# Kernel tuning notes

Hardware: AMD Instinct MI355X
Metric: run time of the kernel (lower is better)

The kernel has to match this reference:

```python
import jax, jax.numpy as jnp
import numpy as np

D = 1024      # model dim
H = 16        # heads
DH = 64       # dim per head (lucidrains default)
DEPTH = 6
MLP = 2048
P = 32
PD = 3 * P * P   # 3072
NC = 1000
B = 4         # packed sequences
N = 640       # tokens per packed sequence (incl. padding)
M = 18        # images per packed sequence
GRID = 8      # image_size // patch_size
SIZES = [(8,8),(8,8),(7,7),(7,7),(6,8),(8,6),(6,6),(5,7),(7,5),(5,5),(4,8),(8,4),(4,6),(6,4),(4,4),(3,5),(5,3),(3,3)]
SCALE = DH ** -0.5


def _pack_meta():
    hs, ws, ids = [], [], []
    for i, (h, w) in enumerate(SIZES):
        hh, ww = np.meshgrid(np.arange(h), np.arange(w), indexing='ij')
        hs.append(hh.ravel()); ws.append(ww.ravel()); ids.append(np.full(h * w, i))
    h = np.concatenate(hs); w = np.concatenate(ws); ii = np.concatenate(ids)
    pad = N - h.shape[0]
    h = np.pad(h, (0, pad)); w = np.pad(w, (0, pad))
    ii = np.pad(ii, (0, pad), constant_values=-1)  # padding tokens form their own block
    return (np.tile(h, (B, 1)).astype(np.int32),
            np.tile(w, (B, 1)).astype(np.int32),
            np.tile(ii, (B, 1)).astype(np.int32))


def _ln(x, g, b, eps=1e-5):
    m = x.mean(-1, keepdims=True)
    v = ((x - m) ** 2).mean(-1, keepdims=True)
    return (x - m) * jax.lax.rsqrt(v + eps) * g + b


def _heads(t):  # [b, n, H*DH] -> [b, H, n, DH]
    return t.reshape(t.shape[0], t.shape[1], H, DH).swapaxes(1, 2)


def _mha(q_in, kv_in, mask, Wq, Wkv, Wo, qn_g, qn_b, kn_g, kn_b):
    # NaViT attention: pre-norm applied by caller to q_in; per-head qk LayerNorm; no biases.
    q = _ln(_heads(q_in @ Wq), qn_g, qn_b)
    k, v = jnp.split(kv_in @ Wkv, 2, axis=-1)
    k = _ln(_heads(k), kn_g, kn_b)
    v = _heads(v)
    dots = jnp.einsum('bhid,bhjd->bhij', q, k) * SCALE
    dots = jnp.where(mask, dots, jnp.finfo(dots.dtype).min)
    o = jnp.einsum('bhij,bhjd->bhid', jax.nn.softmax(dots, axis=-1), v)
    o = o.swapaxes(1, 2).reshape(o.shape[0], -1, H * DH)
    return o @ Wo


def _forward(patches, pe_ln1_g, pe_ln1_b, W_pe, b_pe, pe_ln2_g, pe_ln2_b, pos_h, pos_w,
             ln1_g, ln1_b, qn_g, qn_b, kn_g, kn_b, Wq, Wkv, Wo, ln2_g, ln2_b,
             W1, b1, W2, b2, fin_g, fin_b, pool_q, pl_ln_g, pl_ln_b, pl_qn_g, pl_qn_b,
             pl_kn_g, pl_kn_b, pl_Wq, pl_Wkv, pl_Wo, head_g, head_b, W_head, b_head,
             h_idx, w_idx, image_ids):
    # patch embedding: LN -> Linear -> LN, then factorized 2D pos embed
    x = _ln(patches, pe_ln1_g, pe_ln1_b) @ W_pe + b_pe
    x = _ln(x, pe_ln2_g, pe_ln2_b)
    x = x + pos_h[h_idx] + pos_w[w_idx]
    # block-diagonal attention mask: tokens attend only within their own image
    blk = (image_ids[:, :, None] == image_ids[:, None, :])[:, None]  # [B,1,N,N]
    for l in range(DEPTH):
        xn = _ln(x, ln1_g[l], ln1_b[l])
        x = x + _mha(xn, xn, blk, Wq[l], Wkv[l], Wo[l], qn_g[l], qn_b[l], kn_g[l], kn_b[l])
        xn = _ln(x, ln2_g[l], ln2_b[l])
        x = x + jax.nn.gelu(xn @ W1[l] + b1[l], approximate=False) @ W2[l] + b2[l]
    x = _ln(x, fin_g, fin_b)
    # attention pooling: one learned query per packed image (context NOT re-normed, as in na_vit)
    queries = jnp.broadcast_to(pool_q, (B, M, D))
    qn = _ln(queries, pl_ln_g, pl_ln_b)
    pmask = (jnp.arange(M)[None, :, None] == image_ids[:, None, :])[:, None]  # [B,1,M,N]
    pooled = _mha(qn, x, pmask, pl_Wq, pl_Wkv, pl_Wo, pl_qn_g, pl_qn_b, pl_kn_g, pl_kn_b) + queries
    pooled = pooled.reshape(B * M, D)
    return _ln(pooled, head_g, head_b) @ W_head + b_head  # [B*M, 1000]


def setup_inputs() -> dict:
    key = jax.random.key(0)
    ks = iter(jax.random.split(key, 32))
    h_idx, w_idx, image_ids = _pack_meta()
    f32 = jnp.float32
    d = dict(
        patches=jax.random.normal(next(ks), (B, N, PD), f32),
        pe_ln1_g=jnp.ones((PD,), f32), pe_ln1_b=jnp.zeros((PD,), f32),
        W_pe=0.02 * jax.random.normal(next(ks), (PD, D), f32), b_pe=jnp.zeros((D,), f32),
        pe_ln2_g=jnp.ones((D,), f32), pe_ln2_b=jnp.zeros((D,), f32),
        pos_h=0.02 * jax.random.normal(next(ks), (GRID, D), f32),
        pos_w=0.02 * jax.random.normal(next(ks), (GRID, D), f32),
        ln1_g=jnp.ones((DEPTH, D), f32), ln1_b=jnp.zeros((DEPTH, D), f32),
        qn_g=jnp.ones((DEPTH, DH), f32), qn_b=jnp.zeros((DEPTH, DH), f32),
        kn_g=jnp.ones((DEPTH, DH), f32), kn_b=jnp.zeros((DEPTH, DH), f32),
        Wq=0.02 * jax.random.normal(next(ks), (DEPTH, D, H * DH), f32),
        Wkv=0.02 * jax.random.normal(next(ks), (DEPTH, D, 2 * H * DH), f32),
        Wo=0.02 * jax.random.normal(next(ks), (DEPTH, H * DH, D), f32),
        ln2_g=jnp.ones((DEPTH, D), f32), ln2_b=jnp.zeros((DEPTH, D), f32),
        W1=0.02 * jax.random.normal(next(ks), (DEPTH, D, MLP), f32), b1=jnp.zeros((DEPTH, MLP), f32),
        W2=0.02 * jax.random.normal(next(ks), (DEPTH, MLP, D), f32), b2=jnp.zeros((DEPTH, D), f32),
        fin_g=jnp.ones((D,), f32), fin_b=jnp.zeros((D,), f32),
        pool_q=0.02 * jax.random.normal(next(ks), (D,), f32),
        pl_ln_g=jnp.ones((D,), f32), pl_ln_b=jnp.zeros((D,), f32),
        pl_qn_g=jnp.ones((DH,), f32), pl_qn_b=jnp.zeros((DH,), f32),
        pl_kn_g=jnp.ones((DH,), f32), pl_kn_b=jnp.zeros((DH,), f32),
        pl_Wq=0.02 * jax.random.normal(next(ks), (D, H * DH), f32),
        pl_Wkv=0.02 * jax.random.normal(next(ks), (D, 2 * H * DH), f32),
        pl_Wo=0.02 * jax.random.normal(next(ks), (H * DH, D), f32),
        head_g=jnp.ones((D,), f32), head_b=jnp.zeros((D,), f32),
        W_head=0.02 * jax.random.normal(next(ks), (D, NC), f32), b_head=jnp.zeros((NC,), f32),
        h_idx=jnp.asarray(h_idx), w_idx=jnp.asarray(w_idx), image_ids=jnp.asarray(image_ids),
    )
    return d


def reference(patches, pe_ln1_g, pe_ln1_b, W_pe, b_pe, pe_ln2_g, pe_ln2_b, pos_h, pos_w,
              ln1_g, ln1_b, qn_g, qn_b, kn_g, kn_b, Wq, Wkv, Wo, ln2_g, ln2_b,
              W1, b1, W2, b2, fin_g, fin_b, pool_q, pl_ln_g, pl_ln_b, pl_qn_g, pl_qn_b,
              pl_kn_g, pl_kn_b, pl_Wq, pl_Wkv, pl_Wo, head_g, head_b, W_head, b_head,
              h_idx, w_idx, image_ids):
    return _forward(patches, pe_ln1_g, pe_ln1_b, W_pe, b_pe, pe_ln2_g, pe_ln2_b, pos_h, pos_w,
                    ln1_g, ln1_b, qn_g, qn_b, kn_g, kn_b, Wq, Wkv, Wo, ln2_g, ln2_b,
                    W1, b1, W2, b2, fin_g, fin_b, pool_q, pl_ln_g, pl_ln_b, pl_qn_g, pl_qn_b,
                    pl_kn_g, pl_kn_b, pl_Wq, pl_Wkv, pl_Wo, head_g, head_b, W_head, b_head,
                    h_idx, w_idx, image_ids)
```

## Files before the change

### kernel.cpp

```cpp
#include <hip/hip_runtime.h>
#include <cmath>

constexpr int kB = 4, kN = 640, kD = 1024, kH = 16, kDH = 64;
constexpr int kDepth = 6, kMLP = 2048, kPD = 3072, kNC = 1000, kM = 18;
constexpr float kScale = 0.125f;
constexpr float kNegInf = -3.4028235e38f;

typedef __bf16 bf16;
typedef __attribute__((ext_vector_type(8))) __bf16 bf16x8;
typedef __attribute__((ext_vector_type(4))) __bf16 bf16x4;
typedef __attribute__((ext_vector_type(4))) float f32x4;

#define AS1 __attribute__((address_space(1)))
#define AS3 __attribute__((address_space(3)))

__device__ __forceinline__ void gload16(const void* g, void* l) {
  __builtin_amdgcn_global_load_lds((AS1 void*)g, (AS3 void*)l, 16, 0, 0);
}

constexpr size_t kMEG = 1048576;
constexpr size_t kOffPe = 0;
constexpr size_t kLayer0 = 3 * kMEG;
constexpr size_t kLayerSz = 8 * kMEG;
constexpr size_t kOffPool = kLayer0 + 6 * kLayerSz;
constexpr size_t kOffPlWq = kOffPool;
constexpr size_t kOffPlWkv = kOffPool + 1 * kMEG;
constexpr size_t kOffPlWo = kOffPool + 3 * kMEG;
constexpr size_t kOffHead = kOffPool + 4 * kMEG;

__global__ __launch_bounds__(256) void wt_all_kernel(
    const float* __restrict__ pe, const float* __restrict__ wq,
    const float* __restrict__ wkv, const float* __restrict__ wo,
    const float* __restrict__ w1, const float* __restrict__ w2,
    const float* __restrict__ plq, const float* __restrict__ plkv,
    const float* __restrict__ plo, const float* __restrict__ whead,
    bf16* __restrict__ WTB) {
  const int j = blockIdx.y;
  const float* W;
  size_t doff;
  int K, Nc, Np;
  if (j == 0) {
    W = pe; K = 3072; Nc = 1024; Np = 1024; doff = kOffPe;
  } else if (j < 31) {
    const int l = (j - 1) / 5, w = (j - 1) % 5;
    const size_t lbase = kLayer0 + (size_t)l * kLayerSz;
    switch (w) {
      case 0:  W = wq  + (size_t)l * kMEG;     K = 1024; Nc = 1024; doff = lbase;            break;
      case 1:  W = wkv + (size_t)l * 2 * kMEG; K = 1024; Nc = 2048; doff = lbase + kMEG;     break;
      case 2:  W = wo  + (size_t)l * kMEG;     K = 1024; Nc = 1024; doff = lbase + 3 * kMEG; break;
      case 3:  W = w1  + (size_t)l * 2 * kMEG; K = 1024; Nc = 2048; doff = lbase + 4 * kMEG; break;
      default: W = w2  + (size_t)l * 2 * kMEG; K = 2048; Nc = 1024; doff = lbase + 6 * kMEG; break;
    }
    Np = Nc;
  } else if (j == 31) { W = plq;  K = 1024; Nc = 1024; Np = 1024; doff = kOffPlWq; }
  else if (j == 32)   { W = plkv; K = 1024; Nc = 2048; Np = 2048; doff = kOffPlWkv; }
  else if (j == 33)   { W = plo;  K = 1024; Nc = 1024; Np = 1024; doff = kOffPlWo; }
  else                { W = whead; K = 1024; Nc = 1000; Np = 1024; doff = kOffHead; }
  const int nbx = Np >> 6;
  const int ntiles = nbx * (K >> 6);
  const int tile = blockIdx.x;
  if (tile >= ntiles) return;
  const int n0 = (tile % nbx) * 64, k0 = (tile / nbx) * 64;
  bf16* WT = WTB + doff;
  __shared__ float s[64][65];
  const int tid = threadIdx.x;
  if (n0 + 64 <= Nc) {
#pragma unroll
    for (int i = 0; i < 4; ++i) {
      const int c = i * 256 + tid;
      const int r = c >> 4, cq = c & 15;
      const float4 v = *(const float4*)(W + (size_t)(k0 + r) * Nc + n0 + cq * 4);
      s[r][cq * 4 + 0] = v.x; s[r][cq * 4 + 1] = v.y;
      s[r][cq * 4 + 2] = v.z; s[r][cq * 4 + 3] = v.w;
    }
  } else {
#pragma unroll
    for (int i = 0; i < 4; ++i) {
      const int c = i * 256 + tid;
      const int r = c >> 4, cq = c & 15;
#pragma unroll
      for (int e = 0; e < 4; ++e) {
        const int n = n0 + cq * 4 + e;
        s[r][cq * 4 + e] = (n < Nc) ? W[(size_t)(k0 + r) * Nc + n] : 0.f;
      }
    }
  }
  __syncthreads();
#pragma unroll
  for (int i = 0; i < 2; ++i) {
    const int c = i * 256 + tid;
    const int n = c >> 3, kq = c & 7;
    bf16x8 w;
#pragma unroll
    for (int e = 0; e < 8; ++e) w[e] = (bf16)s[kq * 8 + e][n];
    *(bf16x8*)(WT + (size_t)(n0 + n) * K + k0 + kq * 8) = w;
  }
}

template <typename OT>
__global__ __launch_bounds__(256) void ln_kernel(
    const float* __restrict__ in, OT* __restrict__ out,
    const float* __restrict__ g, const float* __restrict__ b, int K) {
  const int row = blockIdx.x;
  const float* x = in + (size_t)row * K;
  OT* o = out + (size_t)row * K;
  const int K4 = K >> 2;
  float s = 0.f, s2 = 0.f;
  for (int c = threadIdx.x; c < K4; c += 256) {
    const float4 v = ((const float4*)x)[c];
    s += v.x + v.y + v.z + v.w;
    s2 += v.x * v.x + v.y * v.y + v.z * v.z + v.w * v.w;
  }
#pragma unroll
  for (int off = 32; off; off >>= 1) { s += __shfl_down(s, off); s2 += __shfl_down(s2, off); }
  __shared__ float ls[4], ls2[4];
  __shared__ float sm, sr;
  const int wid = threadIdx.x >> 6, lane = threadIdx.x & 63;
  if (lane == 0) { ls[wid] = s; ls2[wid] = s2; }
  __syncthreads();
  if (threadIdx.x == 0) {
    float a = ls[0] + ls[1] + ls[2] + ls[3];
    float a2 = ls2[0] + ls2[1] + ls2[2] + ls2[3];
    float mean = a / K;
    float var = a2 / K - mean * mean;
    sm = mean; sr = rsqrtf(var + 1e-5f);
  }
  __syncthreads();
  const float mean = sm, r = sr;
  for (int c = threadIdx.x; c < K4; c += 256) {
    const float4 v = ((const float4*)x)[c];
    const float4 gv = ((const float4*)g)[c];
    const float4 bv = ((const float4*)b)[c];
    const int d = c * 4;
    o[d + 0] = (OT)((v.x - mean) * r * gv.x + bv.x);
    o[d + 1] = (OT)((v.y - mean) * r * gv.y + bv.y);
    o[d + 2] = (OT)((v.z - mean) * r * gv.z + bv.z);
    o[d + 3] = (OT)((v.w - mean) * r * gv.w + bv.w);
  }
}

__global__ __launch_bounds__(256) void ln_pos_kernel(
    const float* __restrict__ in, float* __restrict__ out,
    const float* __restrict__ g, const float* __restrict__ b,
    const float* __restrict__ ph, const float* __restrict__ pw,
    const int* __restrict__ hi, const int* __restrict__ wi) {
  const int row = blockIdx.x;
  const float* x = in + (size_t)row * kD;
  float* o = out + (size_t)row * kD;
  const int c = threadIdx.x;
  const float4 v = ((const float4*)x)[c];
  float s = v.x + v.y + v.z + v.w;
  float s2 = v.x * v.x + v.y * v.y + v.z * v.z + v.w * v.w;
#pragma unroll
  for (int off = 32; off; off >>= 1) { s += __shfl_down(s, off); s2 += __shfl_down(s2, off); }
  __shared__ float ls[4], ls2[4];
  __shared__ float sm, sr;
  const int wid = threadIdx.x >> 6, lane = threadIdx.x & 63;
  if (lane == 0) { ls[wid] = s; ls2[wid] = s2; }
  __syncthreads();
  if (threadIdx.x == 0) {
    float a = ls[0] + ls[1] + ls[2] + ls[3];
    float a2 = ls2[0] + ls2[1] + ls2[2] + ls2[3];
    float mean = a / kD;
    float var = a2 / kD - mean * mean;
    sm = mean; sr = rsqrtf(var + 1e-5f);
  }
  __syncthreads();
  const float mean = sm, r = sr;
  const float4* phr = (const float4*)(ph + (size_t)hi[row] * kD);
  const float4* pwr = (const float4*)(pw + (size_t)wi[row] * kD);
  const float4 gv = ((const float4*)g)[c];
  const float4 bv = ((const float4*)b)[c];
  const float4 hv = phr[c], wv = pwr[c];
  float4 ov;
  ov.x = (v.x - mean) * r * gv.x + bv.x + hv.x + wv.x;
  ov.y = (v.y - mean) * r * gv.y + bv.y + hv.y + wv.y;
  ov.z = (v.z - mean) * r * gv.z + bv.z + hv.z + wv.z;
  ov.w = (v.w - mean) * r * gv.w + bv.w + hv.w + wv.w;
  ((float4*)o)[c] = ov;
}

__global__ __launch_bounds__(256) void poolq_kernel(
    const float* __restrict__ pq, const float* __restrict__ lg,
    const float* __restrict__ lb, const bf16* __restrict__ WqT,
    const float* __restrict__ qg, const float* __restrict__ qb,
    float* __restrict__ qpool) {
  const int h = blockIdx.x, tid = threadIdx.x;
  __shared__ float qs[1024];
  __shared__ float red[256];
  __shared__ float ls[4], ls2[4];
  __shared__ float sm, sr;
  const float4 v = ((const float4*)pq)[tid];
  float s = v.x + v.y + v.z + v.w;
  float s2 = v.x * v.x + v.y * v.y + v.z * v.z + v.w * v.w;
#pragma unroll
  for (int off = 32; off; off >>= 1) { s += __shfl_down(s, off); s2 += __shfl_down(s2, off); }
  const int wid = tid >> 6, lane = tid & 63;
  if (lane == 0) { ls[wid] = s; ls2[wid] = s2; }
  __syncthreads();
  if (tid == 0) {
    float a = ls[0] + ls[1] + ls[2] + ls[3];
    float a2 = ls2[0] + ls2[1] + ls2[2] + ls2[3];
    float mean = a / kD;
    sm = mean; sr = rsqrtf(a2 / kD - mean * mean + 1e-5f);
  }
  __syncthreads();
  {
    const float mean = sm, r = sr;
    const float4 gv = ((const float4*)lg)[tid];
    const float4 bv = ((const float4*)lb)[tid];
    qs[tid * 4 + 0] = (v.x - mean) * r * gv.x + bv.x;
    qs[tid * 4 + 1] = (v.y - mean) * r * gv.y + bv.y;
    qs[tid * 4 + 2] = (v.z - mean) * r * gv.z + bv.z;
    qs[tid * 4 + 3] = (v.w - mean) * r * gv.w + bv.w;
  }
  __syncthreads();
  const int d = tid & 63, qq = tid >> 6;
  const bf16* wrow = WqT + (size_t)(h * 64 + d) * 1024 + qq * 256;
  const float* qp = qs + qq * 256;
  float part = 0.f;
  for (int k = 0; k < 256; k += 8) {
    const bf16x8 w8 = *(const bf16x8*)(wrow + k);
#pragma unroll
    for (int e = 0; e < 8; ++e) part += qp[k + e] * (float)w8[e];
  }
  red[tid] = part;
  __syncthreads();
  if (tid < 64) {
    const float dot = red[tid] + red[tid + 64] + red[tid + 128] + red[tid + 192];
    float hs = dot, hs2 = dot * dot;
#pragma unroll
    for (int off = 32; off; off >>= 1) { hs += __shfl_xor(hs, off); hs2 += __shfl_xor(hs2, off); }
    const float m = hs * (1.f / kDH);
    const float r = rsqrtf(hs2 * (1.f / kDH) - m * m + 1e-5f);
    qpool[h * 64 + tid] = (dot - m) * r * qg[tid] + qb[tid];
  }
}

template <int NI, bool OUT_BF, bool GELU, bool HLN>
__global__ __launch_bounds__(256) void gemm64_kernel(
    const bf16* __restrict__ A, const bf16* __restrict__ WT,
    float* __restrict__ Cf, bf16* __restrict__ Cb,
    const float* __restrict__ bias, const float* __restrict__ res,
    const float* __restrict__ hg, const float* __restrict__ hb,
    int K, int Ncol, int nbx) {
  constexpr int BN = NI * 32;
  __shared__ __align__(16) bf16 As[2][64 * 64];
  __shared__ __align__(16) bf16 Bs[2][BN * 64];
  const int tid = threadIdx.x, lane = tid & 63, wid = tid >> 6;
  const int wr = wid >> 1, wc = wid & 1;
  const int cpx = gridDim.x >> 3;
  const int swz = (blockIdx.x & 7) * cpx + (blockIdx.x >> 3);
  const int row0 = (swz / nbx) * 64, col0 = (swz % nbx) * BN;
  const int fr = lane & 15, fg = lane >> 4;
  f32x4 acc[2][NI] = {};
  bf16* sA = As[0]; bf16* sB = Bs[0];
  bf16* dA = As[1]; bf16* dB = Bs[1];

  auto stage = [&](bf16* tA, bf16* tB, int kt) {
#pragma unroll
    for (int i = 0; i < 2; ++i) {
      const int c = i * 256 + tid;
      const int r = c >> 3, ci = c & 7;
      gload16(A + (size_t)(row0 + r) * K + kt + ((ci ^ (r & 7)) * 8),
              tA + (i * 256 + wid * 64) * 8);
    }
#pragma unroll
    for (int i = 0; i < NI; ++i) {
      const int c = i * 256 + tid;
      const int r = c >> 3, ci = c & 7;
      gload16(WT + (size_t)(col0 + r) * K + kt + ((ci ^ (r & 7)) * 8),
              tB + (i * 256 + wid * 64) * 8);
    }
  };
  auto compute = [&](const bf16* tA, const bf16* tB) {
#pragma unroll
    for (int kk = 0; kk < 2; ++kk) {
      bf16x8 af[2], bfr[NI];
#pragma unroll
      for (int mi = 0; mi < 2; ++mi) {
        const int r = wr * 32 + mi * 16 + fr;
        af[mi] = *(const bf16x8*)(tA + r * 64 + (((kk * 4 + fg) ^ (r & 7)) * 8));
      }
#pragma unroll
      for (int ni = 0; ni < NI; ++ni) {
        const int r = wc * (NI * 16) + ni * 16 + fr;
        bfr[ni] = *(const bf16x8*)(tB + r * 64 + (((kk * 4 + fg) ^ (r & 7)) * 8));
      }
#pragma unroll
      for (int mi = 0; mi < 2; ++mi)
#pragma unroll
        for (int ni = 0; ni < NI; ++ni)
          acc[mi][ni] = __builtin_amdgcn_mfma_f32_16x16x32_bf16(af[mi], bfr[ni], acc[mi][ni], 0, 0, 0);
    }
  };

  const int NT = K >> 6;
  stage(sA, sB, 0);
  __syncthreads();
  for (int t = 1; t < NT; ++t) {
    stage(dA, dB, t * 64);
    compute(sA, sB);
    __syncthreads();
    bf16* u;
    u = sA; sA = dA; dA = u;
    u = sB; sB = dB; dB = u;
  }
  compute(sA, sB);

  const int rb = row0 + wr * 32 + fg * 4;
  const int cb = col0 + wc * (NI * 16) + fr;
  float hm[2][4], hr[2][4];
  if (HLN) {
#pragma unroll
    for (int mi = 0; mi < 2; ++mi)
#pragma unroll
      for (int r = 0; r < 4; ++r) {
        float s = 0.f, s2 = 0.f;
#pragma unroll
        for (int ni = 0; ni < NI; ++ni) {
          const float v = acc[mi][ni][r];
          s += v; s2 += v * v;
        }
#pragma unroll
        for (int off = 1; off < 16; off <<= 1) {
          s += __shfl_xor(s, off); s2 += __shfl_xor(s2, off);
        }
        const float m = s * (1.f / kDH);
        hm[mi][r] = m;
        hr[mi][r] = rsqrtf(s2 * (1.f / kDH) - m * m + 1e-5f);
      }
  }
  const bool kHalf = HLN && (cb < kD);
#pragma unroll
  for (int mi = 0; mi < 2; ++mi) {
#pragma unroll
    for (int ni = 0; ni < NI; ++ni) {
      const int cc = cb + ni * 16;
      const float bb = bias ? bias[cc] : 0.f;
      const float hgv = HLN ? hg[ni * 16 + fr] : 0.f;
      const float hbv = HLN ? hb[ni * 16 + fr] : 0.f;
#pragma unroll
      for (int r = 0; r < 4; ++r) {
        const int rr = rb + mi * 16 + r;
        float v = acc[mi][ni][r] + bb;
        if (res) v += res[(size_t)rr * Ncol + cc];
        if (GELU) v = 0.5f * v * (1.f + erff(v * 0.70710678118654752f));
        if (HLN && kHalf) v = (v - hm[mi][r]) * hr[mi][r] * hgv + hbv;
        if (OUT_BF) Cb[(size_t)rr * Ncol + cc] = (bf16)v;
        else        Cf[(size_t)rr * Ncol + cc] = v;
      }
    }
  }
}

template <bool OUT_BF>
__global__ __launch_bounds__(256) void gemm_tail_kernel(
    const bf16* __restrict__ A, const bf16* __restrict__ WT,
    float* __restrict__ Cf, bf16* __restrict__ Cb,
    const float* __restrict__ bias, const float* __restrict__ resv,
    int Mr, int K, int Nc, int ldc, int resmode) {
  __shared__ __align__(16) bf16 As[64][40];
  __shared__ __align__(16) bf16 Bs[128][40];
  const int tid = threadIdx.x;
  const int lane = tid & 63, wid = tid >> 6;
  const int row0 = blockIdx.y * 64, col0 = blockIdx.x * 128;
  f32x4 acc[4][2] = {};
  const int am = tid >> 2, ako = (tid & 3) * 8;
  const int fr = lane & 15, fg = (lane >> 4) * 8;
  for (int k0 = 0; k0 < K; k0 += 32) {
    if (row0 + am < Mr)
      *(bf16x8*)&As[am][ako] = *(const bf16x8*)(A + (size_t)(row0 + am) * K + k0 + ako);
    else {
      bf16x8 z = {};
      *(bf16x8*)&As[am][ako] = z;
    }
#pragma unroll
    for (int it = 0; it < 2; ++it) {
      const int c = it * 256 + tid;
      const int n = c >> 2, ko = (c & 3) * 8;
      *(bf16x8*)&Bs[n][ko] = *(const bf16x8*)(WT + (size_t)(col0 + n) * K + k0 + ko);
    }
    __syncthreads();
    bf16x8 af[4], bfr[2];
#pragma unroll
    for (int mi = 0; mi < 4; ++mi) af[mi] = *(const bf16x8*)&As[mi * 16 + fr][fg];
#pragma unroll
    for (int ni = 0; ni < 2; ++ni) bfr[ni] = *(const bf16x8*)&Bs[wid * 32 + ni * 16 + fr][fg];
#pragma unroll
    for (int mi = 0; mi < 4; ++mi)
#pragma unroll
      for (int ni = 0; ni < 2; ++ni)
        acc[mi][ni] = __builtin_amdgcn_mfma_f32_16x16x32_bf16(af[mi], bfr[ni], acc[mi][ni], 0, 0, 0);
    __syncthreads();
  }
  const int r4 = (lane >> 4) * 4;
  const int cc0 = col0 + wid * 32 + (lane & 15);
#pragma unroll
  for (int mi = 0; mi < 4; ++mi) {
#pragma unroll
    for (int ni = 0; ni < 2; ++ni) {
      const int cc = cc0 + ni * 16;
      if (cc >= Nc) continue;
#pragma unroll
      for (int r = 0; r < 4; ++r) {
        const int rr = row0 + mi * 16 + r4 + r;
        if (rr >= Mr) continue;
        float v = acc[mi][ni][r];
        if (bias) v += bias[cc];
        if (resmode == 1) v += resv[(size_t)rr * ldc + cc];
        else if (resmode == 2) v += resv[cc];
        if (OUT_BF) Cb[(size_t)rr * ldc + cc] = (bf16)v;
        else        Cf[(size_t)rr * ldc + cc] = v;
      }
    }
  }
}

__global__ __launch_bounds__(256) void attn_kernel(
    const bf16* __restrict__ qkv, const int* __restrict__ ids,
    const float* __restrict__ qg, const float* __restrict__ qb,
    const float* __restrict__ kg, const float* __restrict__ kb,
    bf16* __restrict__ o) {
  const int h = blockIdx.x, img = blockIdx.y, b = blockIdx.z;
  const int tid = threadIdx.x, lane = tid & 63, wid = tid >> 6;
  __shared__ __align__(16) bf16 Qs[64][72];
  __shared__ __align__(16) bf16 Ks[64][72];
  __shared__ __align__(16) bf16 Vt[64][72];
  __shared__ __align__(16) bf16 Ps[64][72];
  __shared__ int wlo[4], whi[4];
  __shared__ int sLo, sHi;
  {
    const int want = (img < kM) ? img : -1;
    int lo = kN, hi = -1;
    for (int j = tid; j < kN; j += 256) {
      if (ids[b * kN + j] == want) { lo = min(lo, j); hi = max(hi, j); }
    }
#pragma unroll
    for (int off = 32; off; off >>= 1) {
      lo = min(lo, __shfl_xor(lo, off));
      hi = max(hi, __shfl_xor(hi, off));
    }
    if (lane == 0) { wlo[wid] = lo; whi[wid] = hi; }
    __syncthreads();
    if (tid == 0) {
      sLo = min(min(wlo[0], wlo[1]), min(wlo[2], wlo[3]));
      sHi = max(max(whi[0], whi[1]), max(whi[2], whi[3]));
    }
    __syncthreads();
  }
  if (sHi < 0) return;
  const int start = sLo, T = sHi - sLo + 1;
  if (img == kM) {
    for (int j = start + wid; j <= sHi; j += 4)
      o[((size_t)(b * kN + j)) * kD + h * kDH + lane] = (bf16)0.f;
    return;
  }
#pragma unroll
  for (int it = 0; it < 2; ++it) {
    const int ch = it * 256 + tid;
    const int r = ch >> 3, d0 = (ch & 7) * 8;
    if (r < T) {
      const bf16* base = qkv + ((size_t)(b * kN + start + r)) * 3072 + h * kDH + d0;
      const bf16x8 qv = *(const bf16x8*)(base);
      const bf16x8 kv = *(const bf16x8*)(base + 1024);
      const bf16x8 vv = *(const bf16x8*)(base + 2048);
      float qf[8], kf[8];
      float sq = 0.f, sq2 = 0.f, sk = 0.f, sk2 = 0.f;
#pragma unroll
      for (int e = 0; e < 8; ++e) {
        qf[e] = (float)qv[e]; kf[e] = (float)kv[e];
        sq += qf[e]; sq2 += qf[e] * qf[e];
        sk += kf[e]; sk2 += kf[e] * kf[e];
      }
#pragma unroll
      for (int off = 1; off < 8; off <<= 1) {
        sq += __shfl_xor(sq, off); sq2 += __shfl_xor(sq2, off);
        sk += __shfl_xor(sk, off); sk2 += __shfl_xor(sk2, off);
      }
      const float qm = sq * (1.f / 64);
      const float qr = rsqrtf(sq2 * (1.f / 64) - qm * qm + 1e-5f);
      const float km = sk * (1.f / 64);
      const float kr = rsqrtf(sk2 * (1.f / 64) - km * km + 1e-5f);
      bf16x8 qw, kw;
#pragma unroll
      for (int e = 0; e < 8; ++e) {
        qw[e] = (bf16)((qf[e] - qm) * qr * qg[d0 + e] + qb[d0 + e]);
        kw[e] = (bf16)((kf[e] - km) * kr * kg[d0 + e] + kb[d0 + e]);
      }
      *(bf16x8*)&Qs[r][d0] = qw;
      *(bf16x8*)&Ks[r][d0] = kw;
#pragma unroll
      for (int e = 0; e < 8; ++e) Vt[d0 + e][r] = vv[e];
    } else {
      const bf16x8 z = {};
      *(bf16x8*)&Qs[r][d0] = z;
      *(bf16x8*)&Ks[r][d0] = z;
#pragma unroll
      for (int e = 0; e < 8; ++e) Vt[d0 + e][r] = (bf16)0.f;
    }
  }
  __syncthreads();
  const int fr = lane & 15, fg = lane >> 4;
  const int r0 = wid * 16;
  f32x4 sacc[4] = {};
#pragma unroll
  for (int k0 = 0; k0 < 64; k0 += 32) {
    const bf16x8 aq = *(const bf16x8*)&Qs[r0 + fr][k0 + fg * 8];
#pragma unroll
    for (int ni = 0; ni < 4; ++ni) {
      const bf16x8 bk = *(const bf16x8*)&Ks[ni * 16 + fr][k0 + fg * 8];
      sacc[ni] = __builtin_amdgcn_mfma_f32_16x16x32_bf16(aq, bk, sacc[ni], 0, 0, 0);
    }
  }
  float inv[4];
#pragma unroll
  for (int r = 0; r < 4; ++r) {
    float mx = kNegInf;
#pragma unroll
    for (int ni = 0; ni < 4; ++ni) {
      const float s = (ni * 16 + fr < T) ? sacc[ni][r] * kScale : kNegInf;
      sacc[ni][r] = s;
      mx = fmaxf(mx, s);
    }
#pragma unroll
    for (int off = 1; off < 16; off <<= 1) mx = fmaxf(mx, __shfl_xor(mx, off));
    float sum = 0.f;
#pragma unroll
    for (int ni = 0; ni < 4; ++ni) {
      const float p = __expf(sacc[ni][r] - mx);
      sacc[ni][r] = p;
      sum += p;
    }
#pragma unroll
    for (int off = 1; off < 16; off <<= 1) sum += __shfl_xor(sum, off);
    inv[r] = 1.f / sum;
  }
#pragma unroll
  for (int ni = 0; ni < 4; ++ni)
#pragma unroll
    for (int r = 0; r < 4; ++r)
      Ps[r0 + fg * 4 + r][ni * 16 + fr] = (bf16)sacc[ni][r];
  f32x4 oacc[4] = {};
#pragma unroll
  for (int k0 = 0; k0 < 64; k0 += 32) {
    const bf16x8 ap = *(const bf16x8*)&Ps[r0 + fr][k0 + fg * 8];
#pragma unroll
    for (int ni = 0; ni < 4; ++ni) {
      const bf16x8 bv = *(const bf16x8*)&Vt[ni * 16 + fr][k0 + fg * 8];
      oacc[ni] = __builtin_amdgcn_mfma_f32_16x16x32_bf16(ap, bv, oacc[ni], 0, 0, 0);
    }
  }
#pragma unroll
  for (int r = 0; r < 4; ++r) {
    const int i = r0 + fg * 4 + r;
    if (i < T) {
      const size_t orow = ((size_t)(b * kN + start + i)) * kD + h * kDH;
      const float iv = inv[r];
#pragma unroll
      for (int ni = 0; ni < 4; ++ni)
        o[orow + ni * 16 + fr] = (bf16)(oacc[ni][r] * iv);
    }
  }
}

__global__ __launch_bounds__(64) void poolattn_kernel(
    const float* __restrict__ qp, const bf16* __restrict__ kv,
    const int* __restrict__ ids, bf16* __restrict__ o) {
  const int blk = blockIdx.x;
  const int h = blk % kH;
  const int bm = blk / kH;
  const int m = bm % kM, b = bm / kM;
  const int lane = threadIdx.x;
  __shared__ float sc[kN];
  __shared__ float qs[kDH];
  qs[lane] = qp[h * kDH + lane];
  __syncthreads();
  float mymax = kNegInf;
  int jmn = kN, jmx = -1;
  for (int j = lane; j < kN; j += 64) {
    const int idj = ids[b * kN + j];
    float s;
    if (idj == m) {
      const bf16* krow = kv + ((size_t)(b * kN + j)) * (2 * kD) + h * kDH;
      float dot = 0.f;
#pragma unroll
      for (int d = 0; d < kDH; ++d) dot += qs[d] * (float)krow[d];
      s = dot * kScale;
      jmn = min(jmn, j); jmx = max(jmx, j);
    } else {
      s = kNegInf;
    }
    sc[j] = s;
    mymax = fmaxf(mymax, s);
  }
#pragma unroll
  for (int off = 32; off; off >>= 1) {
    mymax = fmaxf(mymax, __shfl_xor(mymax, off));
    jmn = min(jmn, __shfl_xor(jmn, off));
    jmx = max(jmx, __shfl_xor(jmx, off));
  }
  const int jlo = jmn, jhi = jmx + 1;
  float mysum = 0.f;
  for (int j = jlo + lane; j < jhi; j += 64) {
    const float p = __expf(sc[j] - mymax);
    sc[j] = p;
    mysum += p;
  }
#pragma unroll
  for (int off = 32; off; off >>= 1) mysum += __shfl_xor(mysum, off);
  const float inv = 1.f / mysum;
  __syncthreads();
  float acc = 0.f;
  const bf16* vptr = kv + ((size_t)(b * kN + jlo)) * (2 * kD) + kD + h * kDH + lane;
  for (int j = jlo; j < jhi; ++j, vptr += 2 * kD) acc += sc[j] * (float)vptr[0];
  o[((size_t)(b * kM + m)) * kD + h * kDH + lane] = (bf16)(acc * inv);
}

extern "C" void kernel_launch(void* const* d_in, const int* in_sizes, int n_in,
                              void* d_out, int out_size, void* d_ws, size_t ws_size,
                              hipStream_t stream) {
  const float* patches  = (const float*)d_in[0];
  const float* pe_ln1_g = (const float*)d_in[1];
  const float* pe_ln1_b = (const float*)d_in[2];
  const float* W_pe     = (const float*)d_in[3];
  const float* b_pe     = (const float*)d_in[4];
  const float* pe_ln2_g = (const float*)d_in[5];
  const float* pe_ln2_b = (const float*)d_in[6];
  const float* pos_h    = (const float*)d_in[7];
  const float* pos_w    = (const float*)d_in[8];
  const float* ln1_g    = (const float*)d_in[9];
  const float* ln1_b    = (const float*)d_in[10];
  const float* qn_g     = (const float*)d_in[11];
  const float* qn_b     = (const float*)d_in[12];
  const float* kn_g     = (const float*)d_in[13];
  const float* kn_b     = (const float*)d_in[14];
  const float* Wq       = (const float*)d_in[15];
  const float* Wkv      = (const float*)d_in[16];
  const float* Wo       = (const float*)d_in[17];
  const float* ln2_g    = (const float*)d_in[18];
  const float* ln2_b    = (const float*)d_in[19];
  const float* W1       = (const float*)d_in[20];
  const float* b1       = (const float*)d_in[21];
  const float* W2       = (const float*)d_in[22];
  const float* b2       = (const float*)d_in[23];
  const float* fin_g    = (const float*)d_in[24];
  const float* fin_b    = (const float*)d_in[25];
  const float* pool_q   = (const float*)d_in[26];
  const float* pl_ln_g  = (const float*)d_in[27];
  const float* pl_ln_b  = (const float*)d_in[28];
  const float* pl_qn_g  = (const float*)d_in[29];
  const float* pl_qn_b  = (const float*)d_in[30];
  const float* pl_kn_g  = (const float*)d_in[31];
  const float* pl_kn_b  = (const float*)d_in[32];
  const float* pl_Wq    = (const float*)d_in[33];
  const float* pl_Wkv   = (const float*)d_in[34];
  const float* pl_Wo    = (const float*)d_in[35];
  const float* head_g   = (const float*)d_in[36];
  const float* head_b   = (const float*)d_in[37];
  const float* W_head   = (const float*)d_in[38];
  const float* b_head   = (const float*)d_in[39];
  const int* h_idx      = (const int*)d_in[40];
  const int* w_idx      = (const int*)d_in[41];
  const int* image_ids  = (const int*)d_in[42];
  float* out = (float*)d_out;

  const size_t SZ = (size_t)kB * kN * kD;
  char* p = (char*)d_ws;
  float* x    = (float*)p;           p += SZ * 4;
  bf16*  xnb  = (bf16*)p;            p += SZ * 2;
  char*  scratch = p;                p += 32u * 1024 * 1024;
  char*  smalls = p;                 p += 1u * 1024 * 1024;
  bf16*  wtbuf = (bf16*)p;
  bf16*  qkvbb = (bf16*)scratch;
  bf16*  attno = (bf16*)(scratch + 16u * 1024 * 1024);
  bf16*  plnb  = (bf16*)scratch;
  float* emb   = (float*)(scratch + 16u * 1024 * 1024);
  bf16*  h1b   = (bf16*)scratch;
  bf16*  kvpoolb = (bf16*)scratch;
  float* qpool   = (float*)smalls;
  bf16*  opoolb  = (bf16*)(smalls + 8192);
  float* pooled  = (float*)(smalls + 8192 + 163840);
  bf16*  pooledn = (bf16*)(smalls + 8192 + 163840 + 327680);

  const int BN = kB * kN;
  const int nbyM = BN / 64;

  wt_all_kernel<<<dim3(768, 35), 256, 0, stream>>>(
      W_pe, Wq, Wkv, Wo, W1, W2, pl_Wq, pl_Wkv, pl_Wo, W_head, wtbuf);

  ln_kernel<bf16><<<BN, 256, 0, stream>>>(patches, plnb, pe_ln1_g, pe_ln1_b, kPD);
  gemm64_kernel<2, false, false, false><<<(kD / 64) * nbyM, 256, 0, stream>>>(
      plnb, wtbuf + kOffPe, emb, nullptr, b_pe, nullptr, nullptr, nullptr, kPD, kD, kD / 64);
  ln_pos_kernel<<<BN, 256, 0, stream>>>(emb, x, pe_ln2_g, pe_ln2_b, pos_h, pos_w, h_idx, w_idx);

  for (int l = 0; l < kDepth; ++l) {
    const bf16* lw = wtbuf + kLayer0 + (size_t)l * kLayerSz;
    ln_kernel<bf16><<<BN, 256, 0, stream>>>(x, xnb, ln1_g + (size_t)l * kD, ln1_b + (size_t)l * kD, kD);
    gemm64_kernel<2, true, false, false><<<(3 * kD / 64) * nbyM, 256, 0, stream>>>(
        xnb, lw, nullptr, qkvbb, nullptr, nullptr, nullptr, nullptr, kD, 3 * kD, 3 * kD / 64);
    attn_kernel<<<dim3(kH, kM + 1, kB), 256, 0, stream>>>(
        qkvbb, image_ids,
        qn_g + (size_t)l * kDH, qn_b + (size_t)l * kDH,
        kn_g + (size_t)l * kDH, kn_b + (size_t)l * kDH, attno);
    gemm64_kernel<2, false, false, false><<<(kD / 64) * nbyM, 256, 0, stream>>>(
        attno, lw + 3 * kMEG, x, nullptr, nullptr, x, nullptr, nullptr, kD, kD, kD / 64);
    ln_kernel<bf16><<<BN, 256, 0, stream>>>(x, xnb, ln2_g + (size_t)l * kD, ln2_b + (size_t)l * kD, kD);
    gemm64_kernel<2, true, true, false><<<(kMLP / 64) * nbyM, 256, 0, stream>>>(
        xnb, lw + 4 * kMEG, nullptr, h1b, b1 + (size_t)l * kMLP, nullptr, nullptr, nullptr, kD, kMLP, kMLP / 64);
    gemm64_kernel<2, false, false, false><<<(kD / 64) * nbyM, 256, 0, stream>>>(
        h1b, lw + 6 * kMEG, x, nullptr, b2 + (size_t)l * kD, x, nullptr, nullptr, kMLP, kD, kD / 64);
  }

  ln_kernel<bf16><<<BN, 256, 0, stream>>>(x, xnb, fin_g, fin_b, kD);

  poolq_kernel<<<kH, 256, 0, stream>>>(
      pool_q, pl_ln_g, pl_ln_b, wtbuf + kOffPlWq, pl_qn_g, pl_qn_b, qpool);
  gemm64_kernel<4, true, false, true><<<(2 * kD / 128) * nbyM, 256, 0, stream>>>(
      xnb, wtbuf + kOffPlWkv, nullptr, kvpoolb, nullptr, nullptr, pl_kn_g, pl_kn_b, kD, 2 * kD, 2 * kD / 128);
  poolattn_kernel<<<kB * kM * kH, 64, 0, stream>>>(qpool, kvpoolb, image_ids, opoolb);
  gemm_tail_kernel<false><<<dim3(8, 2), 256, 0, stream>>>(
      opoolb, wtbuf + kOffPlWo, pooled, nullptr, nullptr, pool_q, kB * kM, kD, kD, kD, 2);

  ln_kernel<bf16><<<kB * kM, 256, 0, stream>>>(pooled, pooledn, head_g, head_b, kD);
  gemm_tail_kernel<false><<<dim3(8, 2), 256, 0, stream>>>(
      pooledn, wtbuf + kOffHead, out, nullptr, b_head, nullptr, kB * kM, kD, kNC, kNC, 0);
}
```

Baseline: 971.0 us.

## Precompute image spans once; simplify weight transpose to per-thread column reads

Adds a small span_kernel that computes each image's token range once per forward pass. The attention and pool-attention kernels now read those spans instead of scanning image_ids in every block, which removes a reduction and two barriers per block. The weight transpose kernel drops the shared-memory tile: each thread now reads one column across 64 rows, with loads coalesced across threads, and writes 128 contiguous bf16 bytes, so fewer blocks are launched. The per-thread strided writes may coalesce worse than the previous layout, and the span buffer adds one more kernel launch.

After: 966.4 us. No clear change (-0.5%).

```diff
diff --git a/kernel.cpp b/kernel.cpp
--- a/kernel.cpp
+++ b/kernel.cpp
@@ -56,45 +56,46 @@
   else if (j == 32)   { W = plkv; K = 1024; Nc = 2048; Np = 2048; doff = kOffPlWkv; }
   else if (j == 33)   { W = plo;  K = 1024; Nc = 1024; Np = 1024; doff = kOffPlWo; }
   else                { W = whead; K = 1024; Nc = 1000; Np = 1024; doff = kOffHead; }
-  const int nbx = Np >> 6;
-  const int ntiles = nbx * (K >> 6);
+  const int nb = Np >> 8;
+  const int ntiles = nb * (K >> 6);
   const int tile = blockIdx.x;
   if (tile >= ntiles) return;
-  const int n0 = (tile % nbx) * 64, k0 = (tile / nbx) * 64;
+  const int n0 = (tile % nb) * 256, k0 = (tile / nb) * 64;
+  const int n = n0 + threadIdx.x;
   bf16* WT = WTB + doff;
-  __shared__ float s[64][65];
-  const int tid = threadIdx.x;
-  if (n0 + 64 <= Nc) {
-#pragma unroll
-    for (int i = 0; i < 4; ++i) {
-      const int c = i * 256 + tid;
-      const int r = c >> 4, cq = c & 15;
-      const float4 v = *(const float4*)(W + (size_t)(k0 + r) * Nc + n0 + cq * 4);
-      s[r][cq * 4 + 0] = v.x; s[r][cq * 4 + 1] = v.y;
-      s[r][cq * 4 + 2] = v.z; s[r][cq * 4 + 3] = v.w;
+  bf16x8 ob[8];
+  if (n < Nc) {
+    const float* src = W + (size_t)k0 * Nc + n;
+#pragma unroll
+    for (int i = 0; i < 8; ++i) {
+#pragma unroll
+      for (int e = 0; e < 8; ++e)
+        ob[i][e] = (bf16)src[(size_t)(i * 8 + e) * Nc];
     }
   } else {
 #pragma unroll
-    for (int i = 0; i < 4; ++i) {
-      const int c = i * 256 + tid;
-      const int r = c >> 4, cq = c & 15;
-#pragma unroll
-      for (int e = 0; e < 4; ++e) {
-        const int n = n0 + cq * 4 + e;
-        s[r][cq * 4 + e] = (n < Nc) ? W[(size_t)(k0 + r) * Nc + n] : 0.f;
-      }
-    }
-  }
-  __syncthreads();
-#pragma unroll
-  for (int i = 0; i < 2; ++i) {
-    const int c = i * 256 + tid;
-    const int n = c >> 3, kq = c & 7;
-    bf16x8 w;
-#pragma unroll
-    for (int e = 0; e < 8; ++e) w[e] = (bf16)s[kq * 8 + e][n];
-    *(bf16x8*)(WT + (size_t)(n0 + n) * K + k0 + kq * 8) = w;
-  }
+    for (int i = 0; i < 8; ++i) ob[i] = bf16x8{};
+  }
+  bf16* dst = WT + (size_t)n * K + k0;
+#pragma unroll
+  for (int i = 0; i < 8; ++i)
+    *(bf16x8*)(dst + i * 8) = ob[i];
+}
+
+__global__ __launch_bounds__(64) void span_kernel(
+    const int* __restrict__ ids, int2* __restrict__ spans) {
+  const int img = blockIdx.x, b = blockIdx.y;
+  const int want = (img < kM) ? img : -1;
+  int lo = kN, hi = -1;
+  for (int j = threadIdx.x; j < kN; j += 64) {
+    if (ids[b * kN + j] == want) { lo = min(lo, j); hi = max(hi, j); }
+  }
+#pragma unroll
+  for (int off = 32; off; off >>= 1) {
+    lo = min(lo, __shfl_xor(lo, off));
+    hi = max(hi, __shfl_xor(hi, off));
+  }
+  if (threadIdx.x == 0) spans[b * (kM + 1) + img] = make_int2(lo, hi);
 }
 
 template <typename OT>
@@ -418,7 +419,7 @@
 }
 
 __global__ __launch_bounds__(256) void attn_kernel(
-    const bf16* __restrict__ qkv, const int* __restrict__ ids,
+    const bf16* __restrict__ qkv, const int2* __restrict__ spans,
     const float* __restrict__ qg, const float* __restrict__ qb,
     const float* __restrict__ kg, const float* __restrict__ kb,
     bf16* __restrict__ o) {
@@ -428,31 +429,11 @@
   __shared__ __align__(16) bf16 Ks[64][72];
   __shared__ __align__(16) bf16 Vt[64][72];
   __shared__ __align__(16) bf16 Ps[64][72];
-  __shared__ int wlo[4], whi[4];
-  __shared__ int sLo, sHi;
-  {
-    const int want = (img < kM) ? img : -1;
-    int lo = kN, hi = -1;
-    for (int j = tid; j < kN; j += 256) {
-      if (ids[b * kN + j] == want) { lo = min(lo, j); hi = max(hi, j); }
-    }
-#pragma unroll
-    for (int off = 32; off; off >>= 1) {
-      lo = min(lo, __shfl_xor(lo, off));
-      hi = max(hi, __shfl_xor(hi, off));
-    }
-    if (lane == 0) { wlo[wid] = lo; whi[wid] = hi; }
-    __syncthreads();
-    if (tid == 0) {
-      sLo = min(min(wlo[0], wlo[1]), min(wlo[2], wlo[3]));
-      sHi = max(max(whi[0], whi[1]), max(whi[2], whi[3]));
-    }
-    __syncthreads();
-  }
-  if (sHi < 0) return;
-  const int start = sLo, T = sHi - sLo + 1;
+  const int2 sp = spans[b * (kM + 1) + img];
+  if (sp.y < 0) return;
+  const int start = sp.x, T = sp.y - sp.x + 1;
   if (img == kM) {
-    for (int j = start + wid; j <= sHi; j += 4)
+    for (int j = start + wid; j <= sp.y; j += 4)
       o[((size_t)(b * kN + j)) * kD + h * kDH + lane] = (bf16)0.f;
     return;
   }
@@ -566,7 +547,7 @@
 
 __global__ __launch_bounds__(64) void poolattn_kernel(
     const float* __restrict__ qp, const bf16* __restrict__ kv,
-    const int* __restrict__ ids, bf16* __restrict__ o) {
+    const int2* __restrict__ spans, bf16* __restrict__ o) {
   const int blk = blockIdx.x;
   const int h = blk % kH;
   const int bm = blk / kH;
@@ -576,31 +557,20 @@
   __shared__ float qs[kDH];
   qs[lane] = qp[h * kDH + lane];
   __syncthreads();
+  const int2 sp = spans[b * (kM + 1) + m];
+  const int jlo = sp.x, jhi = sp.y + 1;
   float mymax = kNegInf;
-  int jmn = kN, jmx = -1;
-  for (int j = lane; j < kN; j += 64) {
-    const int idj = ids[b * kN + j];
-    float s;
-    if (idj == m) {
-      const bf16* krow = kv + ((size_t)(b * kN + j)) * (2 * kD) + h * kDH;
-      float dot = 0.f;
-#pragma unroll
-      for (int d = 0; d < kDH; ++d) dot += qs[d] * (float)krow[d];
-      s = dot * kScale;
-      jmn = min(jmn, j); jmx = max(jmx, j);
-    } else {
-      s = kNegInf;
-    }
+  for (int j = jlo + lane; j < jhi; j += 64) {
+    const bf16* krow = kv + ((size_t)(b * kN + j)) * (2 * kD) + h * kDH;
+    float dot = 0.f;
+#pragma unroll
+    for (int d = 0; d < kDH; ++d) dot += qs[d] * (float)krow[d];
+    const float s = dot * kScale;
     sc[j] = s;
     mymax = fmaxf(mymax, s);
   }
 #pragma unroll
-  for (int off = 32; off; off >>= 1) {
-    mymax = fmaxf(mymax, __shfl_xor(mymax, off));
-    jmn = min(jmn, __shfl_xor(jmn, off));
-    jmx = max(jmx, __shfl_xor(jmx, off));
-  }
-  const int jlo = jmn, jhi = jmx + 1;
+  for (int off = 32; off; off >>= 1) mymax = fmaxf(mymax, __shfl_xor(mymax, off));
   float mysum = 0.f;
   for (int j = jlo + lane; j < jhi; j += 64) {
     const float p = __expf(sc[j] - mymax);
@@ -682,11 +652,13 @@
   bf16*  opoolb  = (bf16*)(smalls + 8192);
   float* pooled  = (float*)(smalls + 8192 + 163840);
   bf16*  pooledn = (bf16*)(smalls + 8192 + 163840 + 327680);
+  int2*  spans   = (int2*)(smalls + 8192 + 163840 + 327680 + 163840);
 
   const int BN = kB * kN;
   const int nbyM = BN / 64;
 
-  wt_all_kernel<<<dim3(768, 35), 256, 0, stream>>>(
+  span_kernel<<<dim3(kM + 1, kB), 64, 0, stream>>>(image_ids, spans);
+  wt_all_kernel<<<dim3(192, 35), 256, 0, stream>>>(
       W_pe, Wq, Wkv, Wo, W1, W2, pl_Wq, pl_Wkv, pl_Wo, W_head, wtbuf);
 
   ln_kernel<bf16><<<BN, 256, 0, stream>>>(patches, plnb, pe_ln1_g, pe_ln1_b, kPD);
@@ -700,7 +672,7 @@
     gemm64_kernel<2, true, false, false><<<(3 * kD / 64) * nbyM, 256, 0, stream>>>(
         xnb, lw, nullptr, qkvbb, nullptr, nullptr, nullptr, nullptr, kD, 3 * kD, 3 * kD / 64);
     attn_kernel<<<dim3(kH, kM + 1, kB), 256, 0, stream>>>(
-        qkvbb, image_ids,
+        qkvbb, spans,
         qn_g + (size_t)l * kDH, qn_b + (size_t)l * kDH,
         kn_g + (size_t)l * kDH, kn_b + (size_t)l * kDH, attno);
     gemm64_kernel<2, false, false, false><<<(kD / 64) * nbyM, 256, 0, stream>>>(
@@ -718,7 +690,7 @@
       pool_q, pl_ln_g, pl_ln_b, wtbuf + kOffPlWq, pl_qn_g, pl_qn_b, qpool);
   gemm64_kernel<4, true, false, true><<<(2 * kD / 128) * nbyM, 256, 0, stream>>>(
       xnb, wtbuf + kOffPlWkv, nullptr, kvpoolb, nullptr, nullptr, pl_kn_g, pl_kn_b, kD, 2 * kD, 2 * kD / 128);
-  poolattn_kernel<<<kB * kM * kH, 64, 0, stream>>>(qpool, kvpoolb, image_ids, opoolb);
+  poolattn_kernel<<<kB * kM * kH, 64, 0, stream>>>(qpool, kvpoolb, spans, opoolb);
   gemm_tail_kernel<false><<<dim3(8, 2), 256, 0, stream>>>(
       opoolb, wtbuf + kOffPlWo, pooled, nullptr, nullptr, pool_q, kB * kM, kD, kD, kD, 2);
 
```
